# Kernel tuning notes

Hardware: AMD Instinct MI355X
Metric: run time of the kernel (lower is better)

Reference implementation:

```python
import jax, jax.numpy as jnp
import numpy as np

SPATIAL_SHAPES = [(58, 100)]  # single level (H, W)
N_HEADS, N_LEVELS, N_POINTS, NUM_CAMS = 8, 1, 8, 6
D_MODEL = 256


def _bilinear_sample(v, loc, h, w):
    # v: (B, h, w, H, d); loc: (B, Lq, H, P, 2) normalized to [0,1]
    # matches F.grid_sample(mode='bilinear', padding_mode='zeros', align_corners=False)
    x = loc[..., 0] * w - 0.5
    y = loc[..., 1] * h - 0.5
    x0 = jnp.floor(x)
    y0 = jnp.floor(y)
    fx = x - x0
    fy = y - y0
    x0i = x0.astype(jnp.int32)
    y0i = y0.astype(jnp.int32)
    B, Hh = v.shape[0], v.shape[3]
    b = jnp.arange(B)[:, None, None, None]
    hd = jnp.arange(Hh)[None, None, :, None]

    def g(yi, xi):
        valid = ((yi >= 0) & (yi < h) & (xi >= 0) & (xi < w)).astype(v.dtype)
        yc = jnp.clip(yi, 0, h - 1)
        xc = jnp.clip(xi, 0, w - 1)
        return v[b, yc, xc, hd] * valid[..., None]  # (B,Lq,H,P,d)

    return (g(y0i, x0i) * ((1 - fy) * (1 - fx))[..., None]
            + g(y0i, x0i + 1) * ((1 - fy) * fx)[..., None]
            + g(y0i + 1, x0i) * (fy * (1 - fx))[..., None]
            + g(y0i + 1, x0i + 1) * (fy * fx)[..., None])


def _ms_deform_attn(value, locs, weights):
    # value: (B, S, H, d); locs: (B,Lq,H,L,P,2); weights: (B,Lq,H,L,P)
    B, S, Hh, d = value.shape
    out = 0.0
    start = 0
    for l, (h, w) in enumerate(SPATIAL_SHAPES):
        v = value[:, start:start + h * w].reshape(B, h, w, Hh, d)
        start += h * w
        samp = _bilinear_sample(v, locs[:, :, :, l], h, w)  # (B,Lq,H,P,d)
        out = out + jnp.einsum('bqhpd,bqhp->bqhd', samp, weights[:, :, :, l])
    return out.reshape(B, -1, Hh * d)


def setup_inputs() -> dict:
    key = jax.random.key(0)
    ks = jax.random.split(key, 12)
    B, Lq, C = 1, 22500, D_MODEL
    S = sum(h * w for h, w in SPATIAL_SHAPES)
    inp = {
        'query': jax.random.normal(ks[0], (B, Lq, C), jnp.float32),
        'reference_points_cam': jax.random.uniform(ks[1], (NUM_CAMS, B, Lq, 4, 2), jnp.float32),
        'bev_mask': jax.random.randint(ks[2], (NUM_CAMS, B, Lq, 4), 0, 2, jnp.int32),
        'value': jax.random.normal(ks[3], (B * NUM_CAMS, S, C), jnp.float32),
        'W_off': jax.random.normal(ks[4], (N_HEADS * N_LEVELS * N_POINTS * 2, C), jnp.float32) * 0.01,
        'b_off': jax.random.normal(ks[5], (N_HEADS * N_LEVELS * N_POINTS * 2,), jnp.float32),
        'W_attn': jax.random.normal(ks[6], (N_HEADS * N_LEVELS * N_POINTS, C), jnp.float32) * 0.02,
        'b_attn': jnp.zeros((N_HEADS * N_LEVELS * N_POINTS,), jnp.float32),
        'W_val': jax.random.normal(ks[7], (C, C), jnp.float32) * (1.0 / np.sqrt(C)),
        'b_val': jnp.zeros((C,), jnp.float32),
        'W_out': jax.random.normal(ks[8], (C, C), jnp.float32) * (1.0 / np.sqrt(C)),
        'b_out': jnp.zeros((C,), jnp.float32),
    }
    return inp


def reference(query, reference_points_cam, bev_mask, value,
              W_off, b_off, W_attn, b_attn, W_val, b_val, W_out, b_out):
    B, Lq, C = query.shape
    d = C // N_HEADS
    D = reference_points_cam.shape[3]  # num_Z_anchors = 4
    S = value.shape[1]

    # value_proj for all cameras; value rows are laid out as b*num_cams + cam
    val = value @ W_val.T + b_val
    val = val.reshape(B, NUM_CAMS, S, N_HEADS, d).transpose(1, 0, 2, 3, 4)  # (cams,B,S,H,d)

    # query-side projections are camera-independent
    off = (query @ W_off.T + b_off).reshape(B, Lq, N_HEADS, N_LEVELS, N_POINTS, 2)
    normalizer = jnp.array([[w, h] for (h, w) in SPATIAL_SHAPES], dtype=query.dtype)  # (L,2)
    off = off / normalizer[None, None, None, :, None, :]
    off = off.reshape(B, Lq, N_HEADS, N_LEVELS, N_POINTS // D, D, 2)

    aw = (query @ W_attn.T + b_attn).reshape(B, Lq, N_HEADS, N_LEVELS * N_POINTS)
    aw = jax.nn.softmax(aw, axis=-1).reshape(B, Lq, N_HEADS, N_LEVELS, N_POINTS)

    vis = (bev_mask.sum(-1) > 0)  # (cams, B, Lq)
    slots = jnp.zeros_like(query)
    for cam in range(NUM_CAMS):  # small fixed camera set
        ref = reference_points_cam[cam][:, :, None, None, None, :, :]  # (B,Lq,1,1,1,D,2)
        locs = (ref + off).reshape(B, Lq, N_HEADS, N_LEVELS, N_POINTS, 2)
        out = _ms_deform_attn(val[cam], locs, aw)  # (B,Lq,C)
        slots = slots + out * vis[cam][..., None].astype(query.dtype)

    count = jnp.maximum(vis.sum(0).astype(query.dtype), 1.0)  # (B,Lq)
    slots = slots / count[..., None]
    return slots @ W_out.T + b_out
```

## Files before the change

kernel.cpp:

```cpp
#include <hip/hip_runtime.h>

#define LQ     22500
#define SPA_H  58
#define SPA_W  100
#define S_TOT  5800
#define NCAMS  6
#define CDIM   256
#define NB_VAL 544
#define NB_Q   352
#define NB_VIS 88

typedef __attribute__((ext_vector_type(8))) _Float16 half8;
typedef __attribute__((ext_vector_type(4))) float f32x4;

__device__ __forceinline__ half8 cvt_f32x8(const float* p) {
  f32x4 a = *(const f32x4*)p;
  f32x4 b = *(const f32x4*)(p + 4);
  half8 r;
  r[0] = (_Float16)a.x; r[1] = (_Float16)a.y; r[2] = (_Float16)a.z; r[3] = (_Float16)a.w;
  r[4] = (_Float16)b.x; r[5] = (_Float16)b.y; r[6] = (_Float16)b.z; r[7] = (_Float16)b.w;
  return r;
}

template<int N, int OUT_MODE, int BSEL>
__device__ __forceinline__ void gemm_body(
    const float* __restrict__ A, const float* __restrict__ W0,
    const float* __restrict__ W1, const float* __restrict__ b0,
    const float* __restrict__ b1, void* __restrict__ Cv, int M, int bid) {
  constexpr int K  = CDIM;
  constexpr int NT = (N / 4) / 16;
  const int lane = threadIdx.x & 63;
  const int wave = threadIdx.x >> 6;
  const int m15  = lane & 15;
  const int quad = lane >> 4;
  const int rowbase = bid * 64;
  const int colbase = wave * (N / 4);

  const float* wp[NT];
  float bv[NT];
#pragma unroll
  for (int t = 0; t < NT; ++t) {
    const int c = colbase + t * 16 + m15;
    if (BSEL == 0) { wp[t] = W0 + (size_t)c * K; bv[t] = b0[c]; }
    else {
      wp[t] = (c < 128) ? (W0 + (size_t)c * K) : (W1 + (size_t)(c - 128) * K);
      bv[t] = (c < 128) ? b0[c] : b1[c - 128];
    }
  }

  f32x4 acc[4][NT];
#pragma unroll
  for (int rt = 0; rt < 4; ++rt)
#pragma unroll
    for (int t = 0; t < NT; ++t) acc[rt][t] = (f32x4){0.f, 0.f, 0.f, 0.f};

#pragma unroll
  for (int kk = 0; kk < K; kk += 32) {
    const int ko = kk + quad * 8;
    half8 a[4], b[NT];
#pragma unroll
    for (int rt = 0; rt < 4; ++rt) {
      int row = rowbase + rt * 16 + m15;
      row = row < M ? row : M - 1;
      a[rt] = cvt_f32x8(A + (size_t)row * K + ko);
    }
#pragma unroll
    for (int t = 0; t < NT; ++t) b[t] = cvt_f32x8(wp[t] + ko);
#pragma unroll
    for (int t = 0; t < NT; ++t)
#pragma unroll
      for (int rt = 0; rt < 4; ++rt)
        acc[rt][t] = __builtin_amdgcn_mfma_f32_16x16x32_f16(a[rt], b[t], acc[rt][t], 0, 0, 0);
  }

#pragma unroll
  for (int rt = 0; rt < 4; ++rt) {
    const int orow = rowbase + rt * 16 + quad * 4;
#pragma unroll
    for (int t = 0; t < NT; ++t) {
      const int col = colbase + t * 16 + m15;
#pragma unroll
      for (int i = 0; i < 4; ++i) {
        const int r = orow + i;
        if (r < M) {
          const float v = acc[rt][t][i] + bv[t];
          if (OUT_MODE == 0) ((float*)Cv)[(size_t)r * N + col] = v;
          else               ((_Float16*)Cv)[(size_t)r * N + col] = (_Float16)v;
        }
      }
    }
  }
}

__device__ __forceinline__ void vis_body(const int* __restrict__ bev,
                                         unsigned char* __restrict__ vm,
                                         float* __restrict__ invc, int idx) {
  if (idx >= LQ) return;
  int cnt = 0; unsigned m = 0;
#pragma unroll
  for (int c = 0; c < NCAMS; ++c) {
    const int4 b4 = *(const int4*)(bev + ((size_t)c * LQ + idx) * 4);
    const int v = (b4.x + b4.y + b4.z + b4.w) > 0 ? 1 : 0;
    m |= (unsigned)v << c; cnt += v;
  }
  vm[idx] = (unsigned char)m;
  invc[idx] = 1.f / (float)(cnt > 0 ? cnt : 1);
}

__global__ __launch_bounds__(256, 2) void fused_front(
    const float* __restrict__ value, const float* __restrict__ query,
    const int* __restrict__ bev,
    const float* __restrict__ W_val, const float* __restrict__ b_val,
    const float* __restrict__ W_off, const float* __restrict__ b_off,
    const float* __restrict__ W_attn, const float* __restrict__ b_attn,
    _Float16* __restrict__ vp, _Float16* __restrict__ qproj,
    unsigned char* __restrict__ vm, float* __restrict__ invc) {
  const int bid = blockIdx.x;
  if (bid < NB_VAL)
    gemm_body<256, 2, 0>(value, W_val, nullptr, b_val, nullptr, vp, NCAMS * S_TOT, bid);
  else if (bid < NB_VAL + NB_Q)
    gemm_body<192, 2, 1>(query, W_off, W_attn, b_off, b_attn, qproj, LQ, bid - NB_VAL);
  else
    vis_body(bev, vm, invc, (bid - NB_VAL - NB_Q) * 256 + (int)threadIdx.x);
}

__global__ __launch_bounds__(256, 2) void out_gemm(
    const float* __restrict__ slots, const float* __restrict__ W_out,
    const float* __restrict__ b_out, float* __restrict__ out) {
  gemm_body<256, 0, 0>(slots, W_out, nullptr, b_out, nullptr, out, LQ, blockIdx.x);
}

template<int PASS0>
__global__ __launch_bounds__(256, 4) void sampler_pass(
    const _Float16* __restrict__ vp,
    const _Float16* __restrict__ qproj,
    const float* __restrict__ ref,
    const unsigned char* __restrict__ vm,
    const float* __restrict__ invc,
    float* __restrict__ slots,
    int cam)
{
  const int t    = threadIdx.x;
  const int ql   = t >> 5;
  const int s    = t & 31;
  const int h    = s >> 2;
  const int quad = s & 3;
  const int q    = blockIdx.x * 8 + ql;
  const bool qok = q < LQ;

  __shared__ float s_off[8][128];
  __shared__ float s_aw[8][64];
  __shared__ float s_ref[8][8];

  if (qok) {
    const _Float16* qp = qproj + (size_t)q * 192;
#pragma unroll
    for (int rep = 0; rep < 6; ++rep) {
      const int j = s + rep * 32;
      const float v = (float)qp[j];
      if (j < 128) s_off[ql][j] = v * ((j & 1) ? (1.f / 58.f) : (1.f / 100.f));
      else         s_aw[ql][j - 128] = v;
    }
    if (s < 8) s_ref[ql][s] = ref[((size_t)cam * LQ + q) * 8 + s];
  }
  __syncthreads();

  const bool vis = qok && ((vm[q] >> cam) & 1);
  float acc[8];
#pragma unroll
  for (int i = 0; i < 8; ++i) acc[i] = 0.f;

  if (vis) {
    float w8[8];
    float m = -1e30f;
#pragma unroll
    for (int p = 0; p < 8; ++p) m = fmaxf(m, s_aw[ql][h * 8 + p]);
    float ssum = 0.f;
#pragma unroll
    for (int p = 0; p < 8; ++p) { w8[p] = __expf(s_aw[ql][h * 8 + p] - m); ssum += w8[p]; }
    const float inv = 1.f / ssum;
#pragma unroll
    for (int p = 0; p < 8; ++p) w8[p] *= inv;

    const _Float16* vpc = vp + (size_t)cam * (S_TOT * CDIM) + h * 32 + quad * 8;
#pragma unroll 2
    for (int p = 0; p < 8; ++p) {
      const int z = p & 3;
      const float x = (s_ref[ql][z * 2 + 0] + s_off[ql][(h * 8 + p) * 2 + 0]) * 100.f - 0.5f;
      const float y = (s_ref[ql][z * 2 + 1] + s_off[ql][(h * 8 + p) * 2 + 1]) * 58.f - 0.5f;
      const float x0f = floorf(x), y0f = floorf(y);
      const float fx = x - x0f, fy = y - y0f;
      const int x0 = (int)x0f, y0 = (int)y0f;
      const int x1 = x0 + 1,  y1 = y0 + 1;
      const float wgt = w8[p];
      const float gx0 = 1.f - fx, gx1 = fx;
      const float gy0 = (1.f - fy) * wgt, gy1 = fy * wgt;
      const float vx0 = ((unsigned)x0 < SPA_W) ? 1.f : 0.f;
      const float vx1 = ((unsigned)x1 < SPA_W) ? 1.f : 0.f;
      const float vy0 = ((unsigned)y0 < SPA_H) ? 1.f : 0.f;
      const float vy1 = ((unsigned)y1 < SPA_H) ? 1.f : 0.f;
      const float w00 = gy0 * gx0 * (vy0 * vx0);
      const float w01 = gy0 * gx1 * (vy0 * vx1);
      const float w10 = gy1 * gx0 * (vy1 * vx0);
      const float w11 = gy1 * gx1 * (vy1 * vx1);
      const int x0c = min(max(x0, 0), SPA_W - 1);
      const int x1c = min(max(x1, 0), SPA_W - 1);
      const int y0c = min(max(y0, 0), SPA_H - 1);
      const int y1c = min(max(y1, 0), SPA_H - 1);
      const int r0 = y0c * SPA_W, r1 = y1c * SPA_W;
      const _Float16* p00 = vpc + ((size_t)(r0 + x0c) << 8);
      const _Float16* p01 = vpc + ((size_t)(r0 + x1c) << 8);
      const _Float16* p10 = vpc + ((size_t)(r1 + x0c) << 8);
      const _Float16* p11 = vpc + ((size_t)(r1 + x1c) << 8);
      half8 a00 = *(const half8*)p00;
      half8 a01 = *(const half8*)p01;
      half8 a10 = *(const half8*)p10;
      half8 a11 = *(const half8*)p11;
#pragma unroll
      for (int i = 0; i < 8; ++i) {
        float v = acc[i];
        v = fmaf(w00, (float)a00[i], v);
        v = fmaf(w01, (float)a01[i], v);
        v = fmaf(w10, (float)a10[i], v);
        v = fmaf(w11, (float)a11[i], v);
        acc[i] = v;
      }
    }
  }

  if (qok) {
    const float sc = invc[q];
    float* sp = slots + (size_t)q * CDIM + h * 32 + quad * 8;
    if (PASS0) {
      f32x4 o0, o1;
#pragma unroll
      for (int i = 0; i < 4; ++i) { o0[i] = acc[i] * sc; o1[i] = acc[4 + i] * sc; }
      *(f32x4*)sp = o0;
      *(f32x4*)(sp + 4) = o1;
    } else if (vis) {
      f32x4 o0 = *(const f32x4*)sp;
      f32x4 o1 = *(const f32x4*)(sp + 4);
#pragma unroll
      for (int i = 0; i < 4; ++i) { o0[i] += acc[i] * sc; o1[i] += acc[4 + i] * sc; }
      *(f32x4*)sp = o0;
      *(f32x4*)(sp + 4) = o1;
    }
  }
}

extern "C" void kernel_launch(void* const* d_in, const int* in_sizes, int n_in,
                              void* d_out, int out_size, void* d_ws, size_t ws_size,
                              hipStream_t stream) {
  const float* query  = (const float*)d_in[0];
  const float* refpts = (const float*)d_in[1];
  const int*   bev    = (const int*)d_in[2];
  const float* value  = (const float*)d_in[3];
  const float* W_off  = (const float*)d_in[4];
  const float* b_off  = (const float*)d_in[5];
  const float* W_attn = (const float*)d_in[6];
  const float* b_attn = (const float*)d_in[7];
  const float* W_val  = (const float*)d_in[8];
  const float* b_val  = (const float*)d_in[9];
  const float* W_out  = (const float*)d_in[10];
  const float* b_out  = (const float*)d_in[11];

  char* ws = (char*)d_ws;
  _Float16*      vp    = (_Float16*)(ws + 0);
  _Float16*      qproj = (_Float16*)(ws + 17817600);
  float*         slots = (float*)   (ws + 26457600);
  unsigned char* vm    = (unsigned char*)(ws + 49497600);
  float*         invc  = (float*)   (ws + 49520128);

  fused_front<<<NB_VAL + NB_Q + NB_VIS, 256, 0, stream>>>(
      value, query, bev, W_val, b_val, W_off, b_off, W_attn, b_attn,
      vp, qproj, vm, invc);

  sampler_pass<1><<<(LQ + 7) / 8, 256, 0, stream>>>(vp, qproj, refpts, vm, invc, slots, 0);
  for (int cam = 1; cam < NCAMS; ++cam)
    sampler_pass<0><<<(LQ + 7) / 8, 256, 0, stream>>>(vp, qproj, refpts, vm, invc, slots, cam);

  out_gemm<<<NB_Q, 256, 0, stream>>>(slots, W_out, b_out, (float*)d_out);
}
```

Measured before the change: 381.0 us.

## Fuse softmax and scaling into GEMM epilogues and pipeline sampler taps

The attention-weight softmax and the offset normalisation move into the query-projection GEMM epilogue, which now writes fp16 offsets and fp32 weights. The per-query 1/count scaling moves into the output GEMM, which reads slots from the output buffer in place after a barrier. The sampler computes visibility from bev directly and fully unrolls the 8 taps so each tap's loads overlap the previous tap's FMAs. GEMM row tiles shrink from 64 to 32 to launch more blocks. This removes repeated softmax work across six camera passes and the extra slots buffer, at the cost of more register pressure in the sampler and smaller GEMM tiles with less reuse.

```diff
diff --git a/kernel.cpp b/kernel.cpp
--- a/kernel.cpp
+++ b/kernel.cpp
@@ -6,12 +6,15 @@
 #define S_TOT  5800
 #define NCAMS  6
 #define CDIM   256
-#define NB_VAL 544
-#define NB_Q   352
+#define NB_VAL 1088
+#define NB_Q   704
 #define NB_VIS 88
+#define NB_OUT 704
 
 typedef __attribute__((ext_vector_type(8))) _Float16 half8;
+typedef __attribute__((ext_vector_type(4))) _Float16 half4;
 typedef __attribute__((ext_vector_type(4))) float f32x4;
+typedef __attribute__((ext_vector_type(2))) float f32x2;
 
 __device__ __forceinline__ half8 cvt_f32x8(const float* p) {
   f32x4 a = *(const f32x4*)p;
@@ -26,14 +29,17 @@
 __device__ __forceinline__ void gemm_body(
     const float* __restrict__ A, const float* __restrict__ W0,
     const float* __restrict__ W1, const float* __restrict__ b0,
-    const float* __restrict__ b1, void* __restrict__ Cv, int M, int bid) {
+    const float* __restrict__ b1, void* __restrict__ outA,
+    float* __restrict__ outB, const float* __restrict__ rowscale,
+    int M, int bid)
+{
   constexpr int K  = CDIM;
   constexpr int NT = (N / 4) / 16;
   const int lane = threadIdx.x & 63;
   const int wave = threadIdx.x >> 6;
   const int m15  = lane & 15;
   const int quad = lane >> 4;
-  const int rowbase = bid * 64;
+  const int rowbase = bid * 32;
   const int colbase = wave * (N / 4);
 
   const float* wp[NT];
@@ -48,18 +54,18 @@
     }
   }
 
-  f32x4 acc[4][NT];
-#pragma unroll
-  for (int rt = 0; rt < 4; ++rt)
+  f32x4 acc[2][NT];
+#pragma unroll
+  for (int rt = 0; rt < 2; ++rt)
 #pragma unroll
     for (int t = 0; t < NT; ++t) acc[rt][t] = (f32x4){0.f, 0.f, 0.f, 0.f};
 
 #pragma unroll
   for (int kk = 0; kk < K; kk += 32) {
     const int ko = kk + quad * 8;
-    half8 a[4], b[NT];
-#pragma unroll
-    for (int rt = 0; rt < 4; ++rt) {
+    half8 a[2], b[NT];
+#pragma unroll
+    for (int rt = 0; rt < 2; ++rt) {
       int row = rowbase + rt * 16 + m15;
       row = row < M ? row : M - 1;
       a[rt] = cvt_f32x8(A + (size_t)row * K + ko);
@@ -69,23 +75,69 @@
 #pragma unroll
     for (int t = 0; t < NT; ++t)
 #pragma unroll
-      for (int rt = 0; rt < 4; ++rt)
+      for (int rt = 0; rt < 2; ++rt)
         acc[rt][t] = __builtin_amdgcn_mfma_f32_16x16x32_f16(a[rt], b[t], acc[rt][t], 0, 0, 0);
   }
 
-#pragma unroll
-  for (int rt = 0; rt < 4; ++rt) {
+  if (OUT_MODE == 0) __syncthreads();
+
+  float rs[2][4];
+  if (OUT_MODE == 0) {
+#pragma unroll
+    for (int rt = 0; rt < 2; ++rt)
+#pragma unroll
+      for (int i = 0; i < 4; ++i) {
+        int r = rowbase + rt * 16 + quad * 4 + i;
+        rs[rt][i] = rowscale[r < M ? r : M - 1];
+      }
+  }
+
+#pragma unroll
+  for (int rt = 0; rt < 2; ++rt) {
     const int orow = rowbase + rt * 16 + quad * 4;
 #pragma unroll
     for (int t = 0; t < NT; ++t) {
       const int col = colbase + t * 16 + m15;
-#pragma unroll
-      for (int i = 0; i < 4; ++i) {
-        const int r = orow + i;
-        if (r < M) {
-          const float v = acc[rt][t][i] + bv[t];
-          if (OUT_MODE == 0) ((float*)Cv)[(size_t)r * N + col] = v;
-          else               ((_Float16*)Cv)[(size_t)r * N + col] = (_Float16)v;
+      if (OUT_MODE == 3) {
+        if (col >= 128) {
+#pragma unroll
+          for (int i = 0; i < 4; ++i) {
+            const float v = acc[rt][t][i] + bv[t];
+            float mx = v;
+            mx = fmaxf(mx, __shfl_xor(mx, 1, 64));
+            mx = fmaxf(mx, __shfl_xor(mx, 2, 64));
+            mx = fmaxf(mx, __shfl_xor(mx, 4, 64));
+            const float e = __expf(v - mx);
+            float sm = e;
+            sm += __shfl_xor(sm, 1, 64);
+            sm += __shfl_xor(sm, 2, 64);
+            sm += __shfl_xor(sm, 4, 64);
+            const int r = orow + i;
+            if (r < M) outB[(size_t)r * 64 + (col - 128)] = e / sm;
+          }
+        } else {
+          const float sc = (col & 1) ? (1.f / SPA_H) : (1.f / SPA_W);
+#pragma unroll
+          for (int i = 0; i < 4; ++i) {
+            const int r = orow + i;
+            if (r < M)
+              ((_Float16*)outA)[(size_t)r * 128 + col] =
+                  (_Float16)((acc[rt][t][i] + bv[t]) * sc);
+          }
+        }
+      } else if (OUT_MODE == 0) {
+#pragma unroll
+        for (int i = 0; i < 4; ++i) {
+          const int r = orow + i;
+          if (r < M)
+            ((float*)outA)[(size_t)r * N + col] = acc[rt][t][i] * rs[rt][i] + bv[t];
+        }
+      } else {
+#pragma unroll
+        for (int i = 0; i < 4; ++i) {
+          const int r = orow + i;
+          if (r < M)
+            ((_Float16*)outA)[(size_t)r * N + col] = (_Float16)(acc[rt][t][i] + bv[t]);
         }
       }
     }
@@ -93,17 +145,14 @@
 }
 
 __device__ __forceinline__ void vis_body(const int* __restrict__ bev,
-                                         unsigned char* __restrict__ vm,
                                          float* __restrict__ invc, int idx) {
   if (idx >= LQ) return;
-  int cnt = 0; unsigned m = 0;
+  int cnt = 0;
 #pragma unroll
   for (int c = 0; c < NCAMS; ++c) {
     const int4 b4 = *(const int4*)(bev + ((size_t)c * LQ + idx) * 4);
-    const int v = (b4.x + b4.y + b4.z + b4.w) > 0 ? 1 : 0;
-    m |= (unsigned)v << c; cnt += v;
-  }
-  vm[idx] = (unsigned char)m;
+    cnt += (b4.x + b4.y + b4.z + b4.w) > 0 ? 1 : 0;
+  }
   invc[idx] = 1.f / (float)(cnt > 0 ? cnt : 1);
 }
 
@@ -113,30 +162,71 @@
     const float* __restrict__ W_val, const float* __restrict__ b_val,
     const float* __restrict__ W_off, const float* __restrict__ b_off,
     const float* __restrict__ W_attn, const float* __restrict__ b_attn,
-    _Float16* __restrict__ vp, _Float16* __restrict__ qproj,
-    unsigned char* __restrict__ vm, float* __restrict__ invc) {
+    _Float16* __restrict__ vp, _Float16* __restrict__ offb,
+    float* __restrict__ wbuf, float* __restrict__ invc) {
   const int bid = blockIdx.x;
   if (bid < NB_VAL)
-    gemm_body<256, 2, 0>(value, W_val, nullptr, b_val, nullptr, vp, NCAMS * S_TOT, bid);
+    gemm_body<256, 2, 0>(value, W_val, nullptr, b_val, nullptr, vp, nullptr,
+                         nullptr, NCAMS * S_TOT, bid);
   else if (bid < NB_VAL + NB_Q)
-    gemm_body<192, 2, 1>(query, W_off, W_attn, b_off, b_attn, qproj, LQ, bid - NB_VAL);
+    gemm_body<192, 3, 1>(query, W_off, W_attn, b_off, b_attn, offb, wbuf,
+                         nullptr, LQ, bid - NB_VAL);
   else
-    vis_body(bev, vm, invc, (bid - NB_VAL - NB_Q) * 256 + (int)threadIdx.x);
+    vis_body(bev, invc, (bid - NB_VAL - NB_Q) * 256 + (int)threadIdx.x);
 }
 
 __global__ __launch_bounds__(256, 2) void out_gemm(
     const float* __restrict__ slots, const float* __restrict__ W_out,
-    const float* __restrict__ b_out, float* __restrict__ out) {
-  gemm_body<256, 0, 0>(slots, W_out, nullptr, b_out, nullptr, out, LQ, blockIdx.x);
-}
+    const float* __restrict__ b_out, const float* __restrict__ invc,
+    float* __restrict__ out) {
+  gemm_body<256, 0, 0>(slots, W_out, nullptr, b_out, nullptr, out, nullptr,
+                       invc, LQ, blockIdx.x);
+}
+
+#define TAPCOMP(P, S)                                                           \
+  const float x_##S = (s_ref[ql][((P)&3)*2+0] + s_off[ql][(h8+(P))*2+0]) * 100.f - 0.5f; \
+  const float y_##S = (s_ref[ql][((P)&3)*2+1] + s_off[ql][(h8+(P))*2+1]) * 58.f - 0.5f;  \
+  const float x0f_##S = floorf(x_##S), y0f_##S = floorf(y_##S);                 \
+  const float fx_##S = x_##S - x0f_##S, fy_##S = y_##S - y0f_##S;               \
+  const int x0_##S = (int)x0f_##S, y0_##S = (int)y0f_##S;                       \
+  const float wgt_##S = s_w[ql][h8 + (P)];                                      \
+  const float gy0_##S = (1.f - fy_##S) * wgt_##S, gy1_##S = fy_##S * wgt_##S;   \
+  const float vx0_##S = ((unsigned)x0_##S < SPA_W) ? 1.f : 0.f;                 \
+  const float vx1_##S = ((unsigned)(x0_##S + 1) < SPA_W) ? 1.f : 0.f;           \
+  const float vy0_##S = ((unsigned)y0_##S < SPA_H) ? 1.f : 0.f;                 \
+  const float vy1_##S = ((unsigned)(y0_##S + 1) < SPA_H) ? 1.f : 0.f;           \
+  const float w00_##S = gy0_##S * (1.f - fx_##S) * (vy0_##S * vx0_##S);         \
+  const float w01_##S = gy0_##S * fx_##S * (vy0_##S * vx1_##S);                 \
+  const float w10_##S = gy1_##S * (1.f - fx_##S) * (vy1_##S * vx0_##S);         \
+  const float w11_##S = gy1_##S * fx_##S * (vy1_##S * vx1_##S);                 \
+  const int x0c_##S = min(max(x0_##S, 0), SPA_W - 1);                           \
+  const int x1c_##S = min(max(x0_##S + 1, 0), SPA_W - 1);                       \
+  const int y0c_##S = min(max(y0_##S, 0), SPA_H - 1);                           \
+  const int y1c_##S = min(max(y0_##S + 1, 0), SPA_H - 1);                       \
+  const int r0_##S = y0c_##S * SPA_W, r1_##S = y1c_##S * SPA_W;                 \
+  const half8 a00_##S = *(const half8*)(vpc + ((size_t)(r0_##S + x0c_##S) << 8)); \
+  const half8 a01_##S = *(const half8*)(vpc + ((size_t)(r0_##S + x1c_##S) << 8)); \
+  const half8 a10_##S = *(const half8*)(vpc + ((size_t)(r1_##S + x0c_##S) << 8)); \
+  const half8 a11_##S = *(const half8*)(vpc + ((size_t)(r1_##S + x1c_##S) << 8));
+
+#define TAPFMA(S)                                                               \
+  _Pragma("unroll")                                                             \
+  for (int i = 0; i < 8; ++i) {                                                 \
+    float v = acc[i];                                                           \
+    v = fmaf(w00_##S, (float)a00_##S[i], v);                                    \
+    v = fmaf(w01_##S, (float)a01_##S[i], v);                                    \
+    v = fmaf(w10_##S, (float)a10_##S[i], v);                                    \
+    v = fmaf(w11_##S, (float)a11_##S[i], v);                                    \
+    acc[i] = v;                                                                 \
+  }
 
 template<int PASS0>
 __global__ __launch_bounds__(256, 4) void sampler_pass(
     const _Float16* __restrict__ vp,
-    const _Float16* __restrict__ qproj,
+    const _Float16* __restrict__ offb,
+    const float* __restrict__ wbuf,
     const float* __restrict__ ref,
-    const unsigned char* __restrict__ vm,
-    const float* __restrict__ invc,
+    const int* __restrict__ bev,
     float* __restrict__ slots,
     int cam)
 {
@@ -149,99 +239,70 @@
   const bool qok = q < LQ;
 
   __shared__ float s_off[8][128];
-  __shared__ float s_aw[8][64];
+  __shared__ float s_w[8][64];
   __shared__ float s_ref[8][8];
+  __shared__ int   s_vis[8];
 
   if (qok) {
-    const _Float16* qp = qproj + (size_t)q * 192;
-#pragma unroll
-    for (int rep = 0; rep < 6; ++rep) {
-      const int j = s + rep * 32;
-      const float v = (float)qp[j];
-      if (j < 128) s_off[ql][j] = v * ((j & 1) ? (1.f / 58.f) : (1.f / 100.f));
-      else         s_aw[ql][j - 128] = v;
-    }
+    const _Float16* op = offb + (size_t)q * 128;
+    const half4 o4 = *(const half4*)(op + s * 4);
+#pragma unroll
+    for (int k = 0; k < 4; ++k) s_off[ql][s * 4 + k] = (float)o4[k];
+    const f32x2 w2 = *(const f32x2*)(wbuf + (size_t)q * 64 + s * 2);
+    s_w[ql][s * 2]     = w2.x;
+    s_w[ql][s * 2 + 1] = w2.y;
     if (s < 8) s_ref[ql][s] = ref[((size_t)cam * LQ + q) * 8 + s];
   }
+  if (s == 0) {
+    int v = 0;
+    if (qok) {
+      const int4 b4 = *(const int4*)(bev + ((size_t)cam * LQ + q) * 4);
+      v = (b4.x + b4.y + b4.z + b4.w) > 0 ? 1 : 0;
+    }
+    s_vis[ql] = v;
+  }
   __syncthreads();
 
-  const bool vis = qok && ((vm[q] >> cam) & 1);
+  const bool vis = s_vis[ql] != 0;
   float acc[8];
 #pragma unroll
   for (int i = 0; i < 8; ++i) acc[i] = 0.f;
 
+  const int h8 = h * 8;
+  const _Float16* vpc = vp + (size_t)cam * (S_TOT * CDIM) + h * 32 + quad * 8;
+
   if (vis) {
-    float w8[8];
-    float m = -1e30f;
-#pragma unroll
-    for (int p = 0; p < 8; ++p) m = fmaxf(m, s_aw[ql][h * 8 + p]);
-    float ssum = 0.f;
-#pragma unroll
-    for (int p = 0; p < 8; ++p) { w8[p] = __expf(s_aw[ql][h * 8 + p] - m); ssum += w8[p]; }
-    const float inv = 1.f / ssum;
-#pragma unroll
-    for (int p = 0; p < 8; ++p) w8[p] *= inv;
-
-    const _Float16* vpc = vp + (size_t)cam * (S_TOT * CDIM) + h * 32 + quad * 8;
-#pragma unroll 2
-    for (int p = 0; p < 8; ++p) {
-      const int z = p & 3;
-      const float x = (s_ref[ql][z * 2 + 0] + s_off[ql][(h * 8 + p) * 2 + 0]) * 100.f - 0.5f;
-      const float y = (s_ref[ql][z * 2 + 1] + s_off[ql][(h * 8 + p) * 2 + 1]) * 58.f - 0.5f;
-      const float x0f = floorf(x), y0f = floorf(y);
-      const float fx = x - x0f, fy = y - y0f;
-      const int x0 = (int)x0f, y0 = (int)y0f;
-      const int x1 = x0 + 1,  y1 = y0 + 1;
-      const float wgt = w8[p];
-      const float gx0 = 1.f - fx, gx1 = fx;
-      const float gy0 = (1.f - fy) * wgt, gy1 = fy * wgt;
-      const float vx0 = ((unsigned)x0 < SPA_W) ? 1.f : 0.f;
-      const float vx1 = ((unsigned)x1 < SPA_W) ? 1.f : 0.f;
-      const float vy0 = ((unsigned)y0 < SPA_H) ? 1.f : 0.f;
-      const float vy1 = ((unsigned)y1 < SPA_H) ? 1.f : 0.f;
-      const float w00 = gy0 * gx0 * (vy0 * vx0);
-      const float w01 = gy0 * gx1 * (vy0 * vx1);
-      const float w10 = gy1 * gx0 * (vy1 * vx0);
-      const float w11 = gy1 * gx1 * (vy1 * vx1);
-      const int x0c = min(max(x0, 0), SPA_W - 1);
-      const int x1c = min(max(x1, 0), SPA_W - 1);
-      const int y0c = min(max(y0, 0), SPA_H - 1);
-      const int y1c = min(max(y1, 0), SPA_H - 1);
-      const int r0 = y0c * SPA_W, r1 = y1c * SPA_W;
-      const _Float16* p00 = vpc + ((size_t)(r0 + x0c) << 8);
-      const _Float16* p01 = vpc + ((size_t)(r0 + x1c) << 8);
-      const _Float16* p10 = vpc + ((size_t)(r1 + x0c) << 8);
-      const _Float16* p11 = vpc + ((size_t)(r1 + x1c) << 8);
-      half8 a00 = *(const half8*)p00;
-      half8 a01 = *(const half8*)p01;
-      half8 a10 = *(const half8*)p10;
-      half8 a11 = *(const half8*)p11;
-#pragma unroll
-      for (int i = 0; i < 8; ++i) {
-        float v = acc[i];
-        v = fmaf(w00, (float)a00[i], v);
-        v = fmaf(w01, (float)a01[i], v);
-        v = fmaf(w10, (float)a10[i], v);
-        v = fmaf(w11, (float)a11[i], v);
-        acc[i] = v;
-      }
-    }
+    TAPCOMP(0, p0)
+    TAPCOMP(1, p1)
+    TAPFMA(p0)
+    TAPCOMP(2, p2)
+    TAPFMA(p1)
+    TAPCOMP(3, p3)
+    TAPFMA(p2)
+    TAPCOMP(4, p4)
+    TAPFMA(p3)
+    TAPCOMP(5, p5)
+    TAPFMA(p4)
+    TAPCOMP(6, p6)
+    TAPFMA(p5)
+    TAPCOMP(7, p7)
+    TAPFMA(p6)
+    TAPFMA(p7)
   }
 
   if (qok) {
-    const float sc = invc[q];
     float* sp = slots + (size_t)q * CDIM + h * 32 + quad * 8;
     if (PASS0) {
       f32x4 o0, o1;
 #pragma unroll
-      for (int i = 0; i < 4; ++i) { o0[i] = acc[i] * sc; o1[i] = acc[4 + i] * sc; }
+      for (int i = 0; i < 4; ++i) { o0[i] = acc[i]; o1[i] = acc[4 + i]; }
       *(f32x4*)sp = o0;
       *(f32x4*)(sp + 4) = o1;
     } else if (vis) {
       f32x4 o0 = *(const f32x4*)sp;
       f32x4 o1 = *(const f32x4*)(sp + 4);
 #pragma unroll
-      for (int i = 0; i < 4; ++i) { o0[i] += acc[i] * sc; o1[i] += acc[4 + i] * sc; }
+      for (int i = 0; i < 4; ++i) { o0[i] += acc[i]; o1[i] += acc[4 + i]; }
       *(f32x4*)sp = o0;
       *(f32x4*)(sp + 4) = o1;
     }
@@ -265,19 +326,19 @@
   const float* b_out  = (const float*)d_in[11];
 
   char* ws = (char*)d_ws;
-  _Float16*      vp    = (_Float16*)(ws + 0);
-  _Float16*      qproj = (_Float16*)(ws + 17817600);
-  float*         slots = (float*)   (ws + 26457600);
-  unsigned char* vm    = (unsigned char*)(ws + 49497600);
-  float*         invc  = (float*)   (ws + 49520128);
+  _Float16* vp   = (_Float16*)(ws + 0);
+  _Float16* offb = (_Float16*)(ws + 17817600);
+  float*    wbuf = (float*)   (ws + 23577600);
+  float*    invc = (float*)   (ws + 29337600);
+  float* slots = (float*)d_out;
 
   fused_front<<<NB_VAL + NB_Q + NB_VIS, 256, 0, stream>>>(
       value, query, bev, W_val, b_val, W_off, b_off, W_attn, b_attn,
-      vp, qproj, vm, invc);
-
-  sampler_pass<1><<<(LQ + 7) / 8, 256, 0, stream>>>(vp, qproj, refpts, vm, invc, slots, 0);
+      vp, offb, wbuf, invc);
+
+  sampler_pass<1><<<(LQ + 7) / 8, 256, 0, stream>>>(vp, offb, wbuf, refpts, bev, slots, 0);
   for (int cam = 1; cam < NCAMS; ++cam)
-    sampler_pass<0><<<(LQ + 7) / 8, 256, 0, stream>>>(vp, qproj, refpts, vm, invc, slots, cam);
-
-  out_gemm<<<NB_Q, 256, 0, stream>>>(slots, W_out, b_out, (float*)d_out);
-}
+    sampler_pass<0><<<(LQ + 7) / 8, 256, 0, stream>>>(vp, offb, wbuf, refpts, bev, slots, cam);
+
+  out_gemm<<<NB_OUT, 256, 0, stream>>>(slots, W_out, b_out, invc, (float*)d_out);
+}
```

After: 423.9 us. 11.3% more time.

## Fuse six per-camera sampler passes into one kernel with fp16 slots

Applied to the files above, without the earlier changes.

Replaces six per-camera sampler launches, each doing a read-modify-write of fp32 slots, with a single kernel. That kernel loops over cameras, keeps per-query accumulators in registers (24 queries per block) and writes fp16 slots once. The softmax and the offset normalisation move into the query-projection GEMM epilogue, so the sampler reads precomputed weights instead of redoing them per camera. The output GEMM reads fp16 slots directly, which halves slot traffic but adds an extra rounding step and more register pressure in the sampler.

```diff
diff --git a/kernel.cpp b/kernel.cpp
--- a/kernel.cpp
+++ b/kernel.cpp
@@ -9,9 +9,14 @@
 #define NB_VAL 544
 #define NB_Q   352
 #define NB_VIS 88
+#define NB_OUT 352
+#define QB     24
+#define NB_SMP 938
 
 typedef __attribute__((ext_vector_type(8))) _Float16 half8;
+typedef __attribute__((ext_vector_type(4))) _Float16 half4;
 typedef __attribute__((ext_vector_type(4))) float f32x4;
+typedef __attribute__((ext_vector_type(2))) float f32x2;
 
 __device__ __forceinline__ half8 cvt_f32x8(const float* p) {
   f32x4 a = *(const f32x4*)p;
@@ -22,11 +27,13 @@
   return r;
 }
 
-template<int N, int OUT_MODE, int BSEL>
+template<int N, int OUT_MODE, int BSEL, bool A_F16>
 __device__ __forceinline__ void gemm_body(
-    const float* __restrict__ A, const float* __restrict__ W0,
+    const void* __restrict__ Av, const float* __restrict__ W0,
     const float* __restrict__ W1, const float* __restrict__ b0,
-    const float* __restrict__ b1, void* __restrict__ Cv, int M, int bid) {
+    const float* __restrict__ b1, void* __restrict__ outA,
+    float* __restrict__ outB, int M, int bid)
+{
   constexpr int K  = CDIM;
   constexpr int NT = (N / 4) / 16;
   const int lane = threadIdx.x & 63;
@@ -62,7 +69,8 @@
     for (int rt = 0; rt < 4; ++rt) {
       int row = rowbase + rt * 16 + m15;
       row = row < M ? row : M - 1;
-      a[rt] = cvt_f32x8(A + (size_t)row * K + ko);
+      if (A_F16) a[rt] = *(const half8*)((const _Float16*)Av + (size_t)row * K + ko);
+      else       a[rt] = cvt_f32x8((const float*)Av + (size_t)row * K + ko);
     }
 #pragma unroll
     for (int t = 0; t < NT; ++t) b[t] = cvt_f32x8(wp[t] + ko);
@@ -79,13 +87,42 @@
 #pragma unroll
     for (int t = 0; t < NT; ++t) {
       const int col = colbase + t * 16 + m15;
-#pragma unroll
-      for (int i = 0; i < 4; ++i) {
-        const int r = orow + i;
-        if (r < M) {
-          const float v = acc[rt][t][i] + bv[t];
-          if (OUT_MODE == 0) ((float*)Cv)[(size_t)r * N + col] = v;
-          else               ((_Float16*)Cv)[(size_t)r * N + col] = (_Float16)v;
+      if (OUT_MODE == 3) {
+        if (col >= 128) {
+#pragma unroll
+          for (int i = 0; i < 4; ++i) {
+            const float v = acc[rt][t][i] + bv[t];
+            float mx = v;
+            mx = fmaxf(mx, __shfl_xor(mx, 1, 64));
+            mx = fmaxf(mx, __shfl_xor(mx, 2, 64));
+            mx = fmaxf(mx, __shfl_xor(mx, 4, 64));
+            const float e = __expf(v - mx);
+            float sm = e;
+            sm += __shfl_xor(sm, 1, 64);
+            sm += __shfl_xor(sm, 2, 64);
+            sm += __shfl_xor(sm, 4, 64);
+            const int r = orow + i;
+            if (r < M) outB[(size_t)r * 64 + (col - 128)] = e / sm;
+          }
+        } else {
+          const float sc = (col & 1) ? (1.f / SPA_H) : (1.f / SPA_W);
+#pragma unroll
+          for (int i = 0; i < 4; ++i) {
+            const int r = orow + i;
+            if (r < M)
+              ((_Float16*)outA)[(size_t)r * 128 + col] =
+                  (_Float16)((acc[rt][t][i] + bv[t]) * sc);
+          }
+        }
+      } else {
+#pragma unroll
+        for (int i = 0; i < 4; ++i) {
+          const int r = orow + i;
+          if (r < M) {
+            const float v = acc[rt][t][i] + bv[t];
+            if (OUT_MODE == 0) ((float*)outA)[(size_t)r * N + col] = v;
+            else               ((_Float16*)outA)[(size_t)r * N + col] = (_Float16)v;
+          }
         }
       }
     }
@@ -113,137 +150,179 @@
     const float* __restrict__ W_val, const float* __restrict__ b_val,
     const float* __restrict__ W_off, const float* __restrict__ b_off,
     const float* __restrict__ W_attn, const float* __restrict__ b_attn,
-    _Float16* __restrict__ vp, _Float16* __restrict__ qproj,
-    unsigned char* __restrict__ vm, float* __restrict__ invc) {
+    _Float16* __restrict__ vp, _Float16* __restrict__ offb,
+    float* __restrict__ wbuf, unsigned char* __restrict__ vm,
+    float* __restrict__ invc) {
   const int bid = blockIdx.x;
   if (bid < NB_VAL)
-    gemm_body<256, 2, 0>(value, W_val, nullptr, b_val, nullptr, vp, NCAMS * S_TOT, bid);
+    gemm_body<256, 2, 0, false>(value, W_val, nullptr, b_val, nullptr, vp,
+                                nullptr, NCAMS * S_TOT, bid);
   else if (bid < NB_VAL + NB_Q)
-    gemm_body<192, 2, 1>(query, W_off, W_attn, b_off, b_attn, qproj, LQ, bid - NB_VAL);
+    gemm_body<192, 3, 1, false>(query, W_off, W_attn, b_off, b_attn, offb,
+                                wbuf, LQ, bid - NB_VAL);
   else
     vis_body(bev, vm, invc, (bid - NB_VAL - NB_Q) * 256 + (int)threadIdx.x);
 }
 
 __global__ __launch_bounds__(256, 2) void out_gemm(
-    const float* __restrict__ slots, const float* __restrict__ W_out,
+    const _Float16* __restrict__ slots, const float* __restrict__ W_out,
     const float* __restrict__ b_out, float* __restrict__ out) {
-  gemm_body<256, 0, 0>(slots, W_out, nullptr, b_out, nullptr, out, LQ, blockIdx.x);
-}
-
-template<int PASS0>
-__global__ __launch_bounds__(256, 4) void sampler_pass(
+  gemm_body<256, 0, 0, true>(slots, W_out, nullptr, b_out, nullptr, out,
+                             nullptr, LQ, blockIdx.x);
+}
+
+__device__ __forceinline__ void sample_cam(
+    float (&acc)[8], const _Float16* __restrict__ vpc,
+    const float* __restrict__ sref, const float* __restrict__ soff,
+    const float* __restrict__ sw)
+{
+#pragma unroll
+  for (int p = 0; p < 8; ++p) {
+    const int z = p & 3;
+    const float x = (sref[z * 2 + 0] + soff[p * 2 + 0]) * 100.f - 0.5f;
+    const float y = (sref[z * 2 + 1] + soff[p * 2 + 1]) * 58.f - 0.5f;
+    const float x0f = floorf(x), y0f = floorf(y);
+    const float fx = x - x0f, fy = y - y0f;
+    const int x0 = (int)x0f, y0 = (int)y0f;
+    const float wgt = sw[p];
+    const float gx0 = 1.f - fx, gx1 = fx;
+    const float gy0 = (1.f - fy) * wgt, gy1 = fy * wgt;
+    const float vx0 = ((unsigned)x0 < SPA_W) ? 1.f : 0.f;
+    const float vx1 = ((unsigned)(x0 + 1) < SPA_W) ? 1.f : 0.f;
+    const float vy0 = ((unsigned)y0 < SPA_H) ? 1.f : 0.f;
+    const float vy1 = ((unsigned)(y0 + 1) < SPA_H) ? 1.f : 0.f;
+    const float w00 = gy0 * gx0 * (vy0 * vx0);
+    const float w01 = gy0 * gx1 * (vy0 * vx1);
+    const float w10 = gy1 * gx0 * (vy1 * vx0);
+    const float w11 = gy1 * gx1 * (vy1 * vx1);
+    const int x0c = min(max(x0, 0), SPA_W - 1);
+    const int x1c = min(max(x0 + 1, 0), SPA_W - 1);
+    const int y0c = min(max(y0, 0), SPA_H - 1);
+    const int y1c = min(max(y0 + 1, 0), SPA_H - 1);
+    const int r0 = y0c * SPA_W, r1 = y1c * SPA_W;
+    const half8 a00 = *(const half8*)(vpc + ((size_t)(r0 + x0c) << 8));
+    const half8 a01 = *(const half8*)(vpc + ((size_t)(r0 + x1c) << 8));
+    const half8 a10 = *(const half8*)(vpc + ((size_t)(r1 + x0c) << 8));
+    const half8 a11 = *(const half8*)(vpc + ((size_t)(r1 + x1c) << 8));
+#pragma unroll
+    for (int i = 0; i < 8; ++i) {
+      float v = acc[i];
+      v = fmaf(w00, (float)a00[i], v);
+      v = fmaf(w01, (float)a01[i], v);
+      v = fmaf(w10, (float)a10[i], v);
+      v = fmaf(w11, (float)a11[i], v);
+      acc[i] = v;
+    }
+  }
+}
+
+__global__ __launch_bounds__(256, 4) void sampler_all(
     const _Float16* __restrict__ vp,
-    const _Float16* __restrict__ qproj,
+    const _Float16* __restrict__ offb,
+    const float* __restrict__ wbuf,
     const float* __restrict__ ref,
     const unsigned char* __restrict__ vm,
     const float* __restrict__ invc,
-    float* __restrict__ slots,
-    int cam)
+    _Float16* __restrict__ slots)
 {
   const int t    = threadIdx.x;
   const int ql   = t >> 5;
   const int s    = t & 31;
   const int h    = s >> 2;
   const int quad = s & 3;
-  const int q    = blockIdx.x * 8 + ql;
-  const bool qok = q < LQ;
-
-  __shared__ float s_off[8][128];
-  __shared__ float s_aw[8][64];
-  __shared__ float s_ref[8][8];
-
-  if (qok) {
-    const _Float16* qp = qproj + (size_t)q * 192;
-#pragma unroll
-    for (int rep = 0; rep < 6; ++rep) {
-      const int j = s + rep * 32;
-      const float v = (float)qp[j];
-      if (j < 128) s_off[ql][j] = v * ((j & 1) ? (1.f / 58.f) : (1.f / 100.f));
-      else         s_aw[ql][j - 128] = v;
-    }
-    if (s < 8) s_ref[ql][s] = ref[((size_t)cam * LQ + q) * 8 + s];
-  }
-  __syncthreads();
-
-  const bool vis = qok && ((vm[q] >> cam) & 1);
-  float acc[8];
-#pragma unroll
-  for (int i = 0; i < 8; ++i) acc[i] = 0.f;
-
-  if (vis) {
-    float w8[8];
-    float m = -1e30f;
-#pragma unroll
-    for (int p = 0; p < 8; ++p) m = fmaxf(m, s_aw[ql][h * 8 + p]);
-    float ssum = 0.f;
-#pragma unroll
-    for (int p = 0; p < 8; ++p) { w8[p] = __expf(s_aw[ql][h * 8 + p] - m); ssum += w8[p]; }
-    const float inv = 1.f / ssum;
-#pragma unroll
-    for (int p = 0; p < 8; ++p) w8[p] *= inv;
-
-    const _Float16* vpc = vp + (size_t)cam * (S_TOT * CDIM) + h * 32 + quad * 8;
-#pragma unroll 2
-    for (int p = 0; p < 8; ++p) {
-      const int z = p & 3;
-      const float x = (s_ref[ql][z * 2 + 0] + s_off[ql][(h * 8 + p) * 2 + 0]) * 100.f - 0.5f;
-      const float y = (s_ref[ql][z * 2 + 1] + s_off[ql][(h * 8 + p) * 2 + 1]) * 58.f - 0.5f;
-      const float x0f = floorf(x), y0f = floorf(y);
-      const float fx = x - x0f, fy = y - y0f;
-      const int x0 = (int)x0f, y0 = (int)y0f;
-      const int x1 = x0 + 1,  y1 = y0 + 1;
-      const float wgt = w8[p];
-      const float gx0 = 1.f - fx, gx1 = fx;
-      const float gy0 = (1.f - fy) * wgt, gy1 = fy * wgt;
-      const float vx0 = ((unsigned)x0 < SPA_W) ? 1.f : 0.f;
-      const float vx1 = ((unsigned)x1 < SPA_W) ? 1.f : 0.f;
-      const float vy0 = ((unsigned)y0 < SPA_H) ? 1.f : 0.f;
-      const float vy1 = ((unsigned)y1 < SPA_H) ? 1.f : 0.f;
-      const float w00 = gy0 * gx0 * (vy0 * vx0);
-      const float w01 = gy0 * gx1 * (vy0 * vx1);
-      const float w10 = gy1 * gx0 * (vy1 * vx0);
-      const float w11 = gy1 * gx1 * (vy1 * vx1);
-      const int x0c = min(max(x0, 0), SPA_W - 1);
-      const int x1c = min(max(x1, 0), SPA_W - 1);
-      const int y0c = min(max(y0, 0), SPA_H - 1);
-      const int y1c = min(max(y1, 0), SPA_H - 1);
-      const int r0 = y0c * SPA_W, r1 = y1c * SPA_W;
-      const _Float16* p00 = vpc + ((size_t)(r0 + x0c) << 8);
-      const _Float16* p01 = vpc + ((size_t)(r0 + x1c) << 8);
-      const _Float16* p10 = vpc + ((size_t)(r1 + x0c) << 8);
-      const _Float16* p11 = vpc + ((size_t)(r1 + x1c) << 8);
-      half8 a00 = *(const half8*)p00;
-      half8 a01 = *(const half8*)p01;
-      half8 a10 = *(const half8*)p10;
-      half8 a11 = *(const half8*)p11;
-#pragma unroll
-      for (int i = 0; i < 8; ++i) {
-        float v = acc[i];
-        v = fmaf(w00, (float)a00[i], v);
-        v = fmaf(w01, (float)a01[i], v);
-        v = fmaf(w10, (float)a10[i], v);
-        v = fmaf(w11, (float)a11[i], v);
-        acc[i] = v;
-      }
-    }
-  }
-
-  if (qok) {
-    const float sc = invc[q];
-    float* sp = slots + (size_t)q * CDIM + h * 32 + quad * 8;
-    if (PASS0) {
-      f32x4 o0, o1;
-#pragma unroll
-      for (int i = 0; i < 4; ++i) { o0[i] = acc[i] * sc; o1[i] = acc[4 + i] * sc; }
-      *(f32x4*)sp = o0;
-      *(f32x4*)(sp + 4) = o1;
-    } else if (vis) {
-      f32x4 o0 = *(const f32x4*)sp;
-      f32x4 o1 = *(const f32x4*)(sp + 4);
-#pragma unroll
-      for (int i = 0; i < 4; ++i) { o0[i] += acc[i] * sc; o1[i] += acc[4 + i] * sc; }
-      *(f32x4*)sp = o0;
-      *(f32x4*)(sp + 4) = o1;
+  const int q0   = blockIdx.x * QB;
+  const int h8   = h * 8;
+  const int chbase = h * 32 + quad * 8;
+
+  __shared__ float s_off[QB][128];
+  __shared__ float s_w[QB][64];
+  __shared__ float s_ref[QB][8];
+  __shared__ float s_invc[QB];
+  __shared__ unsigned char s_vm[QB];
+
+#pragma unroll
+  for (int rep = 0; rep < 3; ++rep) {
+    const int idx = t + rep * 256;
+    const int u = idx >> 5, g = idx & 31;
+    const int qq = min(q0 + u, LQ - 1);
+    const half4 o4 = *(const half4*)(offb + (size_t)qq * 128 + g * 4);
+#pragma unroll
+    for (int k = 0; k < 4; ++k) s_off[u][g * 4 + k] = (float)o4[k];
+  }
+#pragma unroll
+  for (int rep = 0; rep < 3; ++rep) {
+    const int idx = t + rep * 256;
+    const int u = idx >> 5, g = idx & 31;
+    const int qq = min(q0 + u, LQ - 1);
+    const f32x2 w2 = *(const f32x2*)(wbuf + (size_t)qq * 64 + g * 2);
+    s_w[u][g * 2] = w2.x;
+    s_w[u][g * 2 + 1] = w2.y;
+  }
+  if (t < QB) {
+    const int qq = q0 + t;
+    s_vm[t]   = (qq < LQ) ? vm[qq] : (unsigned char)0;
+    s_invc[t] = (qq < LQ) ? invc[qq] : 1.f;
+  }
+
+  float accA[8], accB[8], accC[8];
+#pragma unroll
+  for (int i = 0; i < 8; ++i) { accA[i] = 0.f; accB[i] = 0.f; accC[i] = 0.f; }
+
+  for (int cam = 0; cam < NCAMS; ++cam) {
+    __syncthreads();
+    if (t < QB * 8) {
+      const int u = t >> 3, k = t & 7;
+      const int qq = min(q0 + u, LQ - 1);
+      s_ref[u][k] = ref[((size_t)cam * LQ + qq) * 8 + k];
+    }
+    __syncthreads();
+
+    const _Float16* vpc = vp + (size_t)cam * (S_TOT * CDIM) + chbase;
+    {
+      const int u = ql;
+      if ((s_vm[u] >> cam) & 1)
+        sample_cam(accA, vpc, s_ref[u], &s_off[u][h8 * 2], &s_w[u][h8]);
+    }
+    {
+      const int u = 8 + ql;
+      if ((s_vm[u] >> cam) & 1)
+        sample_cam(accB, vpc, s_ref[u], &s_off[u][h8 * 2], &s_w[u][h8]);
+    }
+    {
+      const int u = 16 + ql;
+      if ((s_vm[u] >> cam) & 1)
+        sample_cam(accC, vpc, s_ref[u], &s_off[u][h8 * 2], &s_w[u][h8]);
+    }
+  }
+
+  {
+    const int qq = q0 + ql;
+    if (qq < LQ) {
+      const float sc = s_invc[ql];
+      half8 o;
+#pragma unroll
+      for (int i = 0; i < 8; ++i) o[i] = (_Float16)(accA[i] * sc);
+      *(half8*)(slots + (size_t)qq * CDIM + chbase) = o;
+    }
+  }
+  {
+    const int qq = q0 + 8 + ql;
+    if (qq < LQ) {
+      const float sc = s_invc[8 + ql];
+      half8 o;
+#pragma unroll
+      for (int i = 0; i < 8; ++i) o[i] = (_Float16)(accB[i] * sc);
+      *(half8*)(slots + (size_t)qq * CDIM + chbase) = o;
+    }
+  }
+  {
+    const int qq = q0 + 16 + ql;
+    if (qq < LQ) {
+      const float sc = s_invc[16 + ql];
+      half8 o;
+#pragma unroll
+      for (int i = 0; i < 8; ++i) o[i] = (_Float16)(accC[i] * sc);
+      *(half8*)(slots + (size_t)qq * CDIM + chbase) = o;
     }
   }
 }
@@ -266,18 +345,17 @@
 
   char* ws = (char*)d_ws;
   _Float16*      vp    = (_Float16*)(ws + 0);
-  _Float16*      qproj = (_Float16*)(ws + 17817600);
-  float*         slots = (float*)   (ws + 26457600);
-  unsigned char* vm    = (unsigned char*)(ws + 49497600);
-  float*         invc  = (float*)   (ws + 49520128);
+  _Float16*      offb  = (_Float16*)(ws + 17817600);
+  float*         wbuf  = (float*)   (ws + 23577600);
+  unsigned char* vm    = (unsigned char*)(ws + 29337600);
+  float*         invc  = (float*)   (ws + 29360128);
+  _Float16*      slots = (_Float16*)(ws + 29450128);
 
   fused_front<<<NB_VAL + NB_Q + NB_VIS, 256, 0, stream>>>(
       value, query, bev, W_val, b_val, W_off, b_off, W_attn, b_attn,
-      vp, qproj, vm, invc);
-
-  sampler_pass<1><<<(LQ + 7) / 8, 256, 0, stream>>>(vp, qproj, refpts, vm, invc, slots, 0);
-  for (int cam = 1; cam < NCAMS; ++cam)
-    sampler_pass<0><<<(LQ + 7) / 8, 256, 0, stream>>>(vp, qproj, refpts, vm, invc, slots, cam);
-
-  out_gemm<<<NB_Q, 256, 0, stream>>>(slots, W_out, b_out, (float*)d_out);
-}
+      vp, offb, wbuf, vm, invc);
+
+  sampler_all<<<NB_SMP, 256, 0, stream>>>(vp, offb, wbuf, refpts, vm, invc, slots);
+
+  out_gemm<<<NB_OUT, 256, 0, stream>>>(slots, W_out, b_out, (float*)d_out);
+}
```

New measurement: 493.9 us. 1.3x slower.
